# Performance work log

Measured on AMD Instinct MI355X. Metric: run time of the kernel, lower is better.

The kernel has to match this reference:

```python
import jax, jax.numpy as jnp
import numpy as np

C = 256
B, H, W = 16, 64, 64
CQK = C // 8


def setup_inputs() -> dict:
    key = jax.random.key(0)
    ks = jax.random.split(key, 8)
    s = 0.02
    return {
        "x": jax.random.normal(ks[0], (B, C, H, W), dtype=jnp.float32),
        "Wq": jax.random.normal(ks[1], (CQK, C), dtype=jnp.float32) * s,
        "bq": jax.random.normal(ks[2], (CQK,), dtype=jnp.float32) * s,
        "Wk": jax.random.normal(ks[3], (CQK, C), dtype=jnp.float32) * s,
        "bk": jax.random.normal(ks[4], (CQK,), dtype=jnp.float32) * s,
        "Wv": jax.random.normal(ks[5], (C, C), dtype=jnp.float32) * s,
        "bv": jax.random.normal(ks[6], (C,), dtype=jnp.float32) * s,
        "gamma": jax.random.normal(ks[7], (1,), dtype=jnp.float32) * 0.1,
    }


def reference(x, Wq, bq, Wk, bk, Wv, bv, gamma):
    b, c, h, w = x.shape
    n = h * w
    xf = x.reshape(b, c, n)  # flatten spatial -> tokens
    # 1x1 convs are per-token linear maps over channels
    q = jnp.einsum('oc,bcn->bon', Wq, xf) + bq[None, :, None]  # [B, C/8, N]
    k = jnp.einsum('oc,bcn->bon', Wk, xf) + bk[None, :, None]  # [B, C/8, N]
    v = jnp.einsum('oc,bcn->bon', Wv, xf) + bv[None, :, None]  # [B, C,   N]
    attn = jnp.einsum('bdi,bdj->bij', q, k)        # [B, N, N] = Q^T K
    attn = jax.nn.softmax(attn, axis=2)            # softmax over keys
    out = jnp.einsum('bcj,bij->bci', v, attn)      # V @ attn^T -> [B, C, N]
    out = out.reshape(b, c, h, w)
    return gamma[0] * out + x
```

## Files before the change

kernel.cpp:

```cpp
#include <hip/hip_runtime.h>
#include <hip/hip_bf16.h>

#define BB   16
#define CCH  256
#define DQK  32
#define NTOK 4096

typedef __attribute__((ext_vector_type(8)))  short short8;
typedef __attribute__((ext_vector_type(4)))  float f32x4;
typedef __attribute__((ext_vector_type(16))) float f32x16;
typedef unsigned short u16t;
typedef unsigned int   u32t;

__device__ __forceinline__ u16t f2bf(float f){
  u32t u = __builtin_bit_cast(u32t, f);
  u += 0x7FFFu + ((u >> 16) & 1u);
  return (u16t)(u >> 16);
}
__device__ __forceinline__ u32t pk2(float a, float b){
  return (u32t)f2bf(a) | ((u32t)f2bf(b) << 16);
}
__device__ __forceinline__ u32t cvtpk(float lo, float hi_){
  u32t d;
  asm("v_cvt_pk_bf16_f32 %0, %1, %2" : "=v"(d) : "v"(lo), "v"(hi_));
  return d;
}
__device__ __forceinline__ float exp2raw(float x){
  float d;
  asm("v_exp_f32 %0, %1" : "=v"(d) : "v"(x));
  return d;
}
__device__ __forceinline__ void lane32swap(u32t& a, u32t& b){
  asm("v_permlane32_swap_b32 %0, %1" : "+v"(a), "+v"(b));
}
__device__ __forceinline__ float swapadd(float x){
  u32t a = __builtin_bit_cast(u32t, x), b = a;
  lane32swap(a, b);
  return __builtin_bit_cast(float, a) + __builtin_bit_cast(float, b);
}
__device__ __forceinline__ void gload16(const void* g, void* l){
  __builtin_amdgcn_global_load_lds(
      (const __attribute__((address_space(1))) void*)g,
      (__attribute__((address_space(3))) void*)l, 16, 0, 0);
}
__device__ __forceinline__ f32x16 zero16(){
  f32x16 z;
  #pragma unroll
  for (int i = 0; i < 16; ++i) z[i] = 0.f;
  return z;
}
#define mfma32(A, B, C) __builtin_amdgcn_mfma_f32_32x32x16_bf16((A), (B), (C), 0, 0, 0)

__global__ __launch_bounds__(256) void k_wconv(const float* __restrict__ Wq,
    const float* __restrict__ Wk, const float* __restrict__ Wv,
    u16t* __restrict__ o){
  const int base = (blockIdx.x * 256 + threadIdx.x) * 4;
  float4 v;
  if (base < 8192)        v = *(const float4*)(Wq + base);
  else if (base < 16384)  v = *(const float4*)(Wk + base - 8192);
  else                    v = *(const float4*)(Wv + base - 16384);
  *(uint2*)(o + base) = make_uint2(pk2(v.x, v.y), pk2(v.z, v.w));
}

__global__ __launch_bounds__(256) void k_proj(const float* __restrict__ x,
    const u16t* __restrict__ Wb,
    const float* __restrict__ bq, const float* __restrict__ bk,
    const float* __restrict__ bv,
    u16t* __restrict__ Q, u16t* __restrict__ K, u16t* __restrict__ V){
  __shared__ __align__(16) u16t xt[32 * 512];
  const int b = blockIdx.y, nb = blockIdx.x * 64;
  const int tid = threadIdx.x;
  const int w = tid >> 6, lane = tid & 63;
  const int lo = lane & 15, g = lane >> 4;

  const float* xb = x + (size_t)b * CCH * NTOK + nb;
  const int cg = tid >> 4, n0 = (tid & 15) * 4;
  #pragma unroll
  for (int rep = 0; rep < 16; ++rep){
    const int c = rep * 16 + cg;
    float4 v = *(const float4*)(xb + (size_t)c * NTOK + n0);
    const int chunkb = (n0 >> 4) * 8 + (c >> 5);
    const int fl = 16 * ((c >> 3) & 3);
    const int e = c & 7;
    xt[chunkb * 512 + ((n0 & 15) + 0 + fl) * 8 + e] = f2bf(v.x);
    xt[chunkb * 512 + ((n0 & 15) + 1 + fl) * 8 + e] = f2bf(v.y);
    xt[chunkb * 512 + ((n0 & 15) + 2 + fl) * 8 + e] = f2bf(v.z);
    xt[chunkb * 512 + ((n0 & 15) + 3 + fl) * 8 + e] = f2bf(v.w);
  }
  __syncthreads();

  #pragma unroll
  for (int ot = 0; ot < 5; ++ot){
    const u16t* Wrow; const float* bias; int ob; int mode;
    if (ot == 0){
      if (w < 2){ Wrow = Wb;        bias = bq; ob = w * 16;       mode = 0; }
      else      { Wrow = Wb + 8192; bias = bk; ob = (w - 2) * 16; mode = 1; }
    } else { Wrow = Wb + 16384; bias = bv; ob = (ot - 1) * 64 + w * 16; mode = 2; }
    const u16t* wp = Wrow + (size_t)(ob + lo) * CCH + g * 8;

    f32x4 acc[4];
    #pragma unroll
    for (int s = 0; s < 4; ++s) acc[s] = (f32x4){0.f, 0.f, 0.f, 0.f};
    #pragma unroll
    for (int kc = 0; kc < CCH; kc += 32){
      const short8 af = *(const short8*)(wp + kc);
      #pragma unroll
      for (int s = 0; s < 4; ++s){
        const short8 bf = *(const short8*)(xt + (s * 8 + (kc >> 5)) * 512 + lane * 8);
        acc[s] = __builtin_amdgcn_mfma_f32_16x16x32_bf16(af, bf, acc[s], 0, 0, 0);
      }
    }
    #pragma unroll
    for (int s = 0; s < 4; ++s){
      #pragma unroll
      for (int r = 0; r < 4; ++r){
        const int o = ob + 4 * g + r;
        const int n = nb + s * 16 + lo;
        float val = acc[s][r] + bias[o];
        if (mode == 0) val *= 1.44269504088896f;
        const u16t h = f2bf(val);
        if (mode == 0)      Q[((size_t)b * NTOK + n) * DQK + o] = h;
        else if (mode == 1) K[((size_t)b * NTOK + n) * DQK + o] = h;
        else                V[((size_t)b * CCH + o) * NTOK + n] = h;
      }
    }
  }
}

__global__ __launch_bounds__(256, 2) void k_attn(
    const u16t* __restrict__ Q, const u16t* __restrict__ K, const u16t* __restrict__ V,
    const float* __restrict__ x, const float* __restrict__ gamma,
    float* __restrict__ out){
  __shared__ __align__(16) u16t KT[2 * 2048];
  __shared__ __align__(16) u16t Vt[2][CCH * 64];
  const int bid = blockIdx.x;
  const int b  = ((bid & 7) << 1) | ((bid >> 3) & 1);
  const int qt = bid >> 4;
  const int tid = threadIdx.x, w = tid >> 6, lane = tid & 63;
  const int ql = lane & 31, hi = lane >> 5;
  const int qg = qt * 128 + w * 32;

  const u16t* Qb = Q + (size_t)b * NTOK * DQK;
  const u16t* Kb = K + (size_t)b * NTOK * DQK;
  const u16t* Vb = V + (size_t)b * CCH * NTOK;

  const short8 qf0 = *(const short8*)(Qb + (size_t)(qg + ql) * DQK + hi * 8);
  const short8 qf1 = *(const short8*)(Qb + (size_t)(qg + ql) * DQK + 16 + hi * 8);

  f32x16 acc[8];
  #pragma unroll
  for (int c = 0; c < 8; ++c) acc[c] = zero16();
  float l = 0.f;

  const int vrow0 = w * 64 + (lane >> 3);
  const int jsrc  = ((lane & 7) ^ (lane >> 3)) * 8;
  const char* vsrc0 = (const char*)Vb + ((size_t)vrow0 * NTOK + jsrc) * 2;
  const size_t kse = (size_t)((w & 1) * 32 + ql) * DQK + (w >> 1) * 16 + hi * 8;
  const char* ksrc0 = (const char*)Kb + kse * 2;
  const int kla = lane * 16;
  int vaddA[4], vaddB[4];
  #pragma unroll
  for (int kt = 0; kt < 4; ++kt){
    vaddA[kt] = ql * 128 + (((kt * 2 + hi) ^ (ql & 7)) * 16);
    vaddB[kt] = vaddA[kt] + 32768;
  }
  const char* ldsV = (const char*)&Vt[0][0];
  const char* ldsK = (const char*)&KT[0];
  u32t pf[4][4];

  #define EXP_RS(S0, S1, RS) \
    { float r0 = 0.f, r1 = 0.f, r2 = 0.f, r3 = 0.f; \
      _Pragma("unroll") \
      for (int r = 0; r < 16; ++r){ S0[r] = exp2raw(S0[r] - 12.0f); } \
      _Pragma("unroll") \
      for (int r = 0; r < 16; ++r){ S1[r] = exp2raw(S1[r] - 12.0f); } \
      _Pragma("unroll") \
      for (int r = 0; r < 4; ++r){ \
        r0 += S0[r]; r1 += S0[r+4]; r2 += S0[r+8]; r3 += S0[r+12]; \
        r0 += S1[r]; r1 += S1[r+4]; r2 += S1[r+8]; r3 += S1[r+12]; } \
      RS = (r0 + r1) + (r2 + r3); }

  #define PACK_PF(S0, S1) \
    { _Pragma("unroll") \
      for (int js = 0; js < 2; ++js){ \
        _Pragma("unroll") \
        for (int t2 = 0; t2 < 2; ++t2){ \
          const int kt_ = js * 2 + t2, bo = 8 * t2; \
          u32t A1, A2, B1, B2; \
          if (js == 0){ \
            A1 = cvtpk(S0[bo+0], S0[bo+1]); A2 = cvtpk(S0[bo+2], S0[bo+3]); \
            B1 = cvtpk(S0[bo+4], S0[bo+5]); B2 = cvtpk(S0[bo+6], S0[bo+7]); \
          } else { \
            A1 = cvtpk(S1[bo+0], S1[bo+1]); A2 = cvtpk(S1[bo+2], S1[bo+3]); \
            B1 = cvtpk(S1[bo+4], S1[bo+5]); B2 = cvtpk(S1[bo+6], S1[bo+7]); \
          } \
          lane32swap(A1, B1); lane32swap(A2, B2); \
          pf[kt_][0] = A1; pf[kt_][1] = A2; pf[kt_][2] = B1; pf[kt_][3] = B2; \
        } } }

  #define PV_STEP(VRD) \
    { _Pragma("unroll") \
      for (int kt_ = 0; kt_ < 4; ++kt_){ \
        const short8 pb_ = __builtin_bit_cast(short8, \
            make_uint4(pf[kt_][0], pf[kt_][1], pf[kt_][2], pf[kt_][3])); \
        const int va_ = (VRD) ? vaddB[kt_] : vaddA[kt_]; \
        _Pragma("unroll") \
        for (int cs = 0; cs < 8; ++cs){ \
          const short8 vf_ = *(const short8*)(ldsV + va_ + cs * 4096); \
          acc[cs] = mfma32(vf_, pb_, acc[cs]); } } }

  #define QK_STEP(KRD, S0, S1) \
    { const char* kb_ = ldsK + (KRD) * 4096; \
      const short8 kf00 = *(const short8*)(kb_ + kla + 0 * 1024); \
      const short8 kf10 = *(const short8*)(kb_ + kla + 1 * 1024); \
      const short8 kf01 = *(const short8*)(kb_ + kla + 2 * 1024); \
      const short8 kf11 = *(const short8*)(kb_ + kla + 3 * 1024); \
      S0 = mfma32(kf00, qf0, zero16()); S0 = mfma32(kf01, qf1, S0); \
      S1 = mfma32(kf10, qf0, zero16()); S1 = mfma32(kf11, qf1, S1); }

  #define ABODY(T, VRD, KRD, KST) { \
      const int t128_ = ((T) + 1) * 128; \
      _Pragma("unroll") \
      for (int i = 0; i < 8; ++i) \
        gload16(vsrc0 + (size_t)i * 65536 + t128_, &Vt[(VRD)^1][w * 4096 + i * 512]); \
      { const int kt2_ = ((T) + 2 <= 63) ? (T) + 2 : 63; \
        gload16(ksrc0 + (size_t)kt2_ * 4096, &KT[(KST) * 2048 + w * 512]); } \
      f32x16 s0, s1; \
      QK_STEP(KRD, s0, s1); \
      PV_STEP(VRD); \
      float rs_; EXP_RS(s0, s1, rs_); \
      l += swapadd(rs_); \
      PACK_PF(s0, s1); \
      __syncthreads(); }

  #pragma unroll
  for (int i = 0; i < 8; ++i)
    gload16(vsrc0 + (size_t)i * 65536, &Vt[0][w * 4096 + i * 512]);
  gload16(ksrc0,        &KT[0 * 2048 + w * 512]);
  gload16(ksrc0 + 4096, &KT[1 * 2048 + w * 512]);
  __syncthreads();

  {
    f32x16 s0, s1;
    QK_STEP(0, s0, s1);
    float rs_; EXP_RS(s0, s1, rs_);
    l = swapadd(rs_);
    PACK_PF(s0, s1);
  }
  __syncthreads();

  for (int t = 0; t < 62; t += 2){
    ABODY(t,     0, 1, 0)
    ABODY(t + 1, 1, 0, 1)
  }
  ABODY(62, 0, 1, 0)
  PV_STEP(1)

  const float inv = 1.0f / l;
  const float gm = gamma[0];
  const int n = qg + ql;
  #pragma unroll
  for (int cs = 0; cs < 8; ++cs){
    #pragma unroll
    for (int r = 0; r < 16; ++r){
      const int c = cs * 32 + (r & 3) + 8 * (r >> 2) + 4 * hi;
      const size_t idx = ((size_t)b * CCH + c) * NTOK + n;
      out[idx] = gm * (acc[cs][r] * inv) + x[idx];
    }
  }
  #undef EXP_RS
  #undef PACK_PF
  #undef PV_STEP
  #undef QK_STEP
  #undef ABODY
}

extern "C" void kernel_launch(void* const* d_in, const int* in_sizes, int n_in,
                              void* d_out, int out_size, void* d_ws, size_t ws_size,
                              hipStream_t stream) {
  const float* x     = (const float*)d_in[0];
  const float* Wq    = (const float*)d_in[1];
  const float* bq    = (const float*)d_in[2];
  const float* Wk    = (const float*)d_in[3];
  const float* bk    = (const float*)d_in[4];
  const float* Wv    = (const float*)d_in[5];
  const float* bv    = (const float*)d_in[6];
  const float* gamma = (const float*)d_in[7];
  float* out = (float*)d_out;

  char* ws = (char*)d_ws;
  u16t* Qw = (u16t*)(ws);
  u16t* Kw = (u16t*)(ws + 4194304);
  u16t* Vw = (u16t*)(ws + 8388608);
  u16t* Wbf = (u16t*)d_out;

  hipLaunchKernelGGL(k_wconv, dim3(80), dim3(256), 0, stream, Wq, Wk, Wv, Wbf);
  hipLaunchKernelGGL(k_proj, dim3(NTOK / 64, BB), dim3(256), 0, stream,
                     x, Wbf, bq, bk, bv, Qw, Kw, Vw);
  hipLaunchKernelGGL(k_attn, dim3(512), dim3(256), 0, stream,
                     Qw, Kw, Vw, x, gamma, out);
}
```

Baseline: 196.3 us.

## Interleave softmax exp with PV MFMA chunks and defer cross-lane row-sum

Splits the PV matmul into eight per-channel-slice chunks and slots a quarter-row of exp2 and row-sum work between each chunk's MFMAs. Scheduling group barriers pin the order of LDS reads, MFMAs and VALU ops so that exponentiation overlaps the matrix pipeline instead of running after it. The per-iteration permlane swap-add of the row sum becomes one swap at the end of the loop. The constant -12 shift before exp2 is also dropped, which saves a subtract per element but adds some risk of overflow if scores grow large.

```diff
diff --git a/kernel.cpp b/kernel.cpp
--- a/kernel.cpp
+++ b/kernel.cpp
@@ -23,11 +23,6 @@
 __device__ __forceinline__ u32t cvtpk(float lo, float hi_){
   u32t d;
   asm("v_cvt_pk_bf16_f32 %0, %1, %2" : "=v"(d) : "v"(lo), "v"(hi_));
-  return d;
-}
-__device__ __forceinline__ float exp2raw(float x){
-  float d;
-  asm("v_exp_f32 %0, %1" : "=v"(d) : "v"(x));
   return d;
 }
 __device__ __forceinline__ void lane32swap(u32t& a, u32t& b){
@@ -168,18 +163,6 @@
   const char* ldsK = (const char*)&KT[0];
   u32t pf[4][4];
 
-  #define EXP_RS(S0, S1, RS) \
-    { float r0 = 0.f, r1 = 0.f, r2 = 0.f, r3 = 0.f; \
-      _Pragma("unroll") \
-      for (int r = 0; r < 16; ++r){ S0[r] = exp2raw(S0[r] - 12.0f); } \
-      _Pragma("unroll") \
-      for (int r = 0; r < 16; ++r){ S1[r] = exp2raw(S1[r] - 12.0f); } \
-      _Pragma("unroll") \
-      for (int r = 0; r < 4; ++r){ \
-        r0 += S0[r]; r1 += S0[r+4]; r2 += S0[r+8]; r3 += S0[r+12]; \
-        r0 += S1[r]; r1 += S1[r+4]; r2 += S1[r+8]; r3 += S1[r+12]; } \
-      RS = (r0 + r1) + (r2 + r3); }
-
   #define PACK_PF(S0, S1) \
     { _Pragma("unroll") \
       for (int js = 0; js < 2; ++js){ \
@@ -198,17 +181,6 @@
           pf[kt_][0] = A1; pf[kt_][1] = A2; pf[kt_][2] = B1; pf[kt_][3] = B2; \
         } } }
 
-  #define PV_STEP(VRD) \
-    { _Pragma("unroll") \
-      for (int kt_ = 0; kt_ < 4; ++kt_){ \
-        const short8 pb_ = __builtin_bit_cast(short8, \
-            make_uint4(pf[kt_][0], pf[kt_][1], pf[kt_][2], pf[kt_][3])); \
-        const int va_ = (VRD) ? vaddB[kt_] : vaddA[kt_]; \
-        _Pragma("unroll") \
-        for (int cs = 0; cs < 8; ++cs){ \
-          const short8 vf_ = *(const short8*)(ldsV + va_ + cs * 4096); \
-          acc[cs] = mfma32(vf_, pb_, acc[cs]); } } }
-
   #define QK_STEP(KRD, S0, S1) \
     { const char* kb_ = ldsK + (KRD) * 4096; \
       const short8 kf00 = *(const short8*)(kb_ + kla + 0 * 1024); \
@@ -217,6 +189,28 @@
       const short8 kf11 = *(const short8*)(kb_ + kla + 3 * 1024); \
       S0 = mfma32(kf00, qf0, zero16()); S0 = mfma32(kf01, qf1, S0); \
       S1 = mfma32(kf10, qf0, zero16()); S1 = mfma32(kf11, qf1, S1); }
+
+  #define ESL(S, B) \
+    { S[(B)+0] = __builtin_amdgcn_exp2f(S[(B)+0]); r0 += S[(B)+0]; \
+      S[(B)+1] = __builtin_amdgcn_exp2f(S[(B)+1]); r1 += S[(B)+1]; \
+      S[(B)+2] = __builtin_amdgcn_exp2f(S[(B)+2]); r2 += S[(B)+2]; \
+      S[(B)+3] = __builtin_amdgcn_exp2f(S[(B)+3]); r3 += S[(B)+3]; }
+
+  #define PVCHUNK(CS, VRD, EXPSLICE) \
+    { const short8 vf0 = *(const short8*)(ldsV + ((VRD)?vaddB[0]:vaddA[0]) + (CS)*4096); \
+      const short8 vf1 = *(const short8*)(ldsV + ((VRD)?vaddB[1]:vaddA[1]) + (CS)*4096); \
+      const short8 vf2 = *(const short8*)(ldsV + ((VRD)?vaddB[2]:vaddA[2]) + (CS)*4096); \
+      const short8 vf3 = *(const short8*)(ldsV + ((VRD)?vaddB[3]:vaddA[3]) + (CS)*4096); \
+      acc[CS] = mfma32(vf0, pb0, acc[CS]); \
+      acc[CS] = mfma32(vf1, pb1, acc[CS]); \
+      acc[CS] = mfma32(vf2, pb2, acc[CS]); \
+      acc[CS] = mfma32(vf3, pb3, acc[CS]); \
+      EXPSLICE \
+      __builtin_amdgcn_sched_group_barrier(0x100, 4, 0); \
+      __builtin_amdgcn_sched_group_barrier(0x8,   4, 0); \
+      __builtin_amdgcn_sched_group_barrier(0x2,  10, 0); }
+
+  #define NOSL
 
   #define ABODY(T, VRD, KRD, KST) { \
       const int t128_ = ((T) + 1) * 128; \
@@ -227,9 +221,20 @@
         gload16(ksrc0 + (size_t)kt2_ * 4096, &KT[(KST) * 2048 + w * 512]); } \
       f32x16 s0, s1; \
       QK_STEP(KRD, s0, s1); \
-      PV_STEP(VRD); \
-      float rs_; EXP_RS(s0, s1, rs_); \
-      l += swapadd(rs_); \
+      const short8 pb0 = __builtin_bit_cast(short8, make_uint4(pf[0][0], pf[0][1], pf[0][2], pf[0][3])); \
+      const short8 pb1 = __builtin_bit_cast(short8, make_uint4(pf[1][0], pf[1][1], pf[1][2], pf[1][3])); \
+      const short8 pb2 = __builtin_bit_cast(short8, make_uint4(pf[2][0], pf[2][1], pf[2][2], pf[2][3])); \
+      const short8 pb3 = __builtin_bit_cast(short8, make_uint4(pf[3][0], pf[3][1], pf[3][2], pf[3][3])); \
+      float r0 = 0.f, r1 = 0.f, r2 = 0.f, r3 = 0.f; \
+      PVCHUNK(0, VRD, ESL(s0, 0)) \
+      PVCHUNK(1, VRD, ESL(s0, 4)) \
+      PVCHUNK(2, VRD, ESL(s0, 8)) \
+      PVCHUNK(3, VRD, ESL(s0, 12)) \
+      PVCHUNK(4, VRD, ESL(s1, 0)) \
+      PVCHUNK(5, VRD, ESL(s1, 4)) \
+      PVCHUNK(6, VRD, ESL(s1, 8)) \
+      PVCHUNK(7, VRD, ESL(s1, 12)) \
+      l += (r0 + r1) + (r2 + r3); \
       PACK_PF(s0, s1); \
       __syncthreads(); }
 
@@ -243,8 +248,10 @@
   {
     f32x16 s0, s1;
     QK_STEP(0, s0, s1);
-    float rs_; EXP_RS(s0, s1, rs_);
-    l = swapadd(rs_);
+    float r0 = 0.f, r1 = 0.f, r2 = 0.f, r3 = 0.f;
+    ESL(s0, 0) ESL(s0, 4) ESL(s0, 8) ESL(s0, 12)
+    ESL(s1, 0) ESL(s1, 4) ESL(s1, 8) ESL(s1, 12)
+    l = (r0 + r1) + (r2 + r3);
     PACK_PF(s0, s1);
   }
   __syncthreads();
@@ -254,9 +261,18 @@
     ABODY(t + 1, 1, 0, 1)
   }
   ABODY(62, 0, 1, 0)
-  PV_STEP(1)
-
-  const float inv = 1.0f / l;
+
+  {
+    const short8 pb0 = __builtin_bit_cast(short8, make_uint4(pf[0][0], pf[0][1], pf[0][2], pf[0][3]));
+    const short8 pb1 = __builtin_bit_cast(short8, make_uint4(pf[1][0], pf[1][1], pf[1][2], pf[1][3]));
+    const short8 pb2 = __builtin_bit_cast(short8, make_uint4(pf[2][0], pf[2][1], pf[2][2], pf[2][3]));
+    const short8 pb3 = __builtin_bit_cast(short8, make_uint4(pf[3][0], pf[3][1], pf[3][2], pf[3][3]));
+    PVCHUNK(0, 1, NOSL) PVCHUNK(1, 1, NOSL) PVCHUNK(2, 1, NOSL) PVCHUNK(3, 1, NOSL)
+    PVCHUNK(4, 1, NOSL) PVCHUNK(5, 1, NOSL) PVCHUNK(6, 1, NOSL) PVCHUNK(7, 1, NOSL)
+  }
+
+  const float lfull = swapadd(l);
+  const float inv = 1.0f / lfull;
   const float gm = gamma[0];
   const int n = qg + ql;
   #pragma unroll
@@ -268,10 +284,11 @@
       out[idx] = gm * (acc[cs][r] * inv) + x[idx];
     }
   }
-  #undef EXP_RS
   #undef PACK_PF
-  #undef PV_STEP
   #undef QK_STEP
+  #undef ESL
+  #undef PVCHUNK
+  #undef NOSL
   #undef ABODY
 }
 
```

Result: faster. 191.4 us (-2.5%).
